# Kernel tuning notes

Hardware: AMD Instinct MI355X
Metric: run time of the kernel (lower is better)

Reference implementation:

```python
import jax, jax.numpy as jnp
import numpy as np

H = 8   # num_heads
K = 2   # num_timescales (hard-coded in module)


def _apply_rope(x, cos, sin):
    # x: [B,T,H,D]; cos/sin: [1,T,1,D/2]; interleaved even/odd pairs
    xp = x.reshape(*x.shape[:-1], -1, 2)
    xr, xi = xp[..., 0], xp[..., 1]
    rr = xr * cos - xi * sin
    ri = xr * sin + xi * cos
    return jnp.stack([rr, ri], axis=-1).reshape(x.shape)


def setup_inputs() -> dict:
    key = jax.random.key(0)
    ks = jax.random.split(key, 11)
    B, T, C = 4, 2048, 1024
    HK = H * K
    s = 0.02  # xavier-ish scale
    return {
        'x': jax.random.normal(ks[0], (B, T, C), jnp.float32),
        'mask': jnp.ones((B, T), jnp.int32),
        'Wq': jax.random.normal(ks[1], (C, C), jnp.float32) * s,
        'Wk': jax.random.normal(ks[2], (C, C), jnp.float32) * s,
        'Wv': jax.random.normal(ks[3], (C, C), jnp.float32) * s,
        'Wb': jax.random.normal(ks[4], (C, HK), jnp.float32) * s,
        'bb': jax.random.normal(ks[5], (HK,), jnp.float32) * 0.5 + 2.0,
        'Wm': jax.random.normal(ks[6], (C, HK), jnp.float32) * s,
        'bm': jax.random.normal(ks[7], (HK,), jnp.float32) * 0.1,
        'Wo': jax.random.normal(ks[8], (C, C), jnp.float32) * s,
        'bo': jnp.zeros((C,), jnp.float32),
    }


def reference(x, mask, Wq, Wk, Wv, Wb, bb, Wm, bm, Wo, bo):
    B, T, C = x.shape
    D = C // H
    q = (x @ Wq).reshape(B, T, H, D)
    k = (x @ Wk).reshape(B, T, H, D)
    v = (x @ Wv).reshape(B, T, H, D)

    # RoPE cache
    inv_freq = 1.0 / (10000.0 ** (jnp.arange(0, D, 2, dtype=jnp.float32) / D))
    freqs = jnp.arange(T, dtype=jnp.float32)[:, None] * inv_freq[None, :]  # [T,D/2]
    cos = jnp.cos(freqs)[None, :, None, :].astype(x.dtype)
    sin = jnp.sin(freqs)[None, :, None, :].astype(x.dtype)
    q = _apply_rope(q, cos, sin)
    k = _apply_rope(k, cos, sin)

    beta = jax.nn.sigmoid((x @ Wb + bb).reshape(B, T, H, K))  # [B,T,H,K]
    mix = jax.nn.softmax((x @ Wm + bm).reshape(B, T, H, K), axis=-1)

    def step(S, ins):
        # S: [B,H,K,D,D]
        q_t, k_t, v_t, b_t, m_t, mk = ins  # [B,H,D],[B,H,D],[B,H,D],[B,H,K],[B,H,K],[B]
        outer = jnp.einsum('bhd,bhe->bhde', k_t, v_t)          # [B,H,D,D]
        S_new = b_t[..., None, None] * S + outer[:, :, None]   # [B,H,K,D,D]
        S = jnp.where(mk[:, None, None, None, None] > 0, S_new, S)
        y_k = jnp.einsum('bhd,bhkde->bhke', q_t, S)            # [B,H,K,D]
        y_t = jnp.sum(y_k * m_t[..., None], axis=2)            # [B,H,D]
        y_t = jnp.where(mk[:, None, None] > 0, y_t, jnp.zeros_like(y_t))
        return S, y_t

    S0 = jnp.zeros((B, H, K, D, D), x.dtype)
    xs = (jnp.swapaxes(q, 0, 1), jnp.swapaxes(k, 0, 1), jnp.swapaxes(v, 0, 1),
          jnp.swapaxes(beta, 0, 1), jnp.swapaxes(mix, 0, 1), mask.T)
    _, ys = jax.lax.scan(step, S0, xs)           # ys: [T,B,H,D]
    y = jnp.swapaxes(ys, 0, 1).reshape(B, T, C)
    return y @ Wo + bo
```

## Files before the change

### kernel.cpp

```cpp
#include <hip/hip_runtime.h>

typedef __attribute__((ext_vector_type(4))) float f32x4;
typedef __attribute__((ext_vector_type(8))) __bf16 bf16x8;

#define T_DIM 2048
#define B_DIM 4
#define C_DIM 1024
#define H_N 8
#define D_H 128
#define M_ROWS 8192
#define MC ((size_t)M_ROWS * C_DIM)
#define LCH 64
#define NCH (T_DIM / LCH)
#define CHSZ (128 * 128)
#define SWE(r) ((((r) ^ ((r) >> 3)) & 7) << 3)

#define GLDS16(g, l) __builtin_amdgcn_global_load_lds( \
    (const __attribute__((address_space(1))) void*)(g), \
    (__attribute__((address_space(3))) void*)(l), 16, 0, 0)

__global__ void rope_table_k(float2* __restrict__ tab) {
    int idx = blockIdx.x * 256 + threadIdx.x;
    if (idx >= T_DIM * 64) return;
    int t = idx >> 6, i = idx & 63;
    float freq = expf(-(2.0f * (float)i / 128.0f) * 9.210340371976184f);
    float a = (float)t * freq;
    tab[idx] = make_float2(cosf(a), sinf(a));
}

__global__ __launch_bounds__(256) void cvt_x_k(const float* __restrict__ in,
                                               __bf16* __restrict__ out) {
    int i = blockIdx.x * 256 + threadIdx.x;
    f32x4 a = ((const f32x4*)in)[i * 2];
    f32x4 b = ((const f32x4*)in)[i * 2 + 1];
    bf16x8 o;
    o[0] = (__bf16)a.x; o[1] = (__bf16)a.y; o[2] = (__bf16)a.z; o[3] = (__bf16)a.w;
    o[4] = (__bf16)b.x; o[5] = (__bf16)b.y; o[6] = (__bf16)b.z; o[7] = (__bf16)b.w;
    ((bf16x8*)out)[i] = o;
}

__global__ __launch_bounds__(256) void wtrans_k(
    const float* __restrict__ W0, const float* __restrict__ W1,
    const float* __restrict__ W2, const float* __restrict__ W3,
    __bf16* __restrict__ out) {
    const float* W = blockIdx.z == 0 ? W0 : blockIdx.z == 1 ? W1 :
                     blockIdx.z == 2 ? W2 : W3;
    __bf16* o = out + (size_t)blockIdx.z * C_DIM * C_DIM;
    __shared__ float t[64][65];
    int tid = threadIdx.x;
    int r0 = blockIdx.y * 64, c0 = blockIdx.x * 64;
    #pragma unroll
    for (int it = 0; it < 4; ++it) {
        int idx = it * 256 + tid;
        int r = idx >> 4, c4 = (idx & 15) * 4;
        f32x4 v = *(const f32x4*)(W + (size_t)(r0 + r) * C_DIM + c0 + c4);
        t[r][c4] = v.x; t[r][c4 + 1] = v.y; t[r][c4 + 2] = v.z; t[r][c4 + 3] = v.w;
    }
    __syncthreads();
    #pragma unroll
    for (int it = 0; it < 2; ++it) {
        int idx = it * 256 + tid;
        int n = idx >> 3, k8 = (idx & 7) * 8;
        bf16x8 ov;
        #pragma unroll
        for (int j = 0; j < 8; ++j) ov[j] = (__bf16)t[k8 + j][n];
        *(bf16x8*)(o + (size_t)(c0 + n) * C_DIM + r0 + k8) = ov;
    }
}

__global__ __launch_bounds__(256) void wbm_trans_k(
    const float* __restrict__ Wb, const float* __restrict__ Wm,
    __bf16* __restrict__ WbmT) {
    int n = blockIdx.x;
    int col = n & 15;
    const float* W = (n < 16) ? Wb : Wm;
    for (int k = threadIdx.x; k < C_DIM; k += 256)
        WbmT[(size_t)n * C_DIM + k] = (__bf16)W[(size_t)k * 16 + col];
}

__global__ __launch_bounds__(256) void betamix_mfma(
    const __bf16* __restrict__ xb, const __bf16* __restrict__ WbmT,
    const float* __restrict__ bb, const float* __restrict__ bm,
    float* __restrict__ beta, float* __restrict__ mix) {
    __shared__ __bf16 As[32 * 64];

    int tid = threadIdx.x;
    int w = tid >> 6, lane = tid & 63;
    int lr = lane & 15, lg = lane >> 4;
    int ifr = w >> 1, j = w & 1;
    int rows0 = blockIdx.x * 32;

    int srow = tid >> 3;
    int sg = (tid & 7) ^ (srow & 7);
    size_t aoff = (size_t)(rows0 + srow) * C_DIM + sg * 8;
    char* ldsb = (char*)As + w * 64 * 16;

    f32x4 acc = {};
    const __bf16* Wrow = WbmT + (size_t)(j * 16 + lr) * C_DIM;

    for (int k0 = 0; k0 < C_DIM; k0 += 64) {
        __syncthreads();
        GLDS16(xb + aoff + k0, ldsb);
        __syncthreads();
        #pragma unroll
        for (int ss = 0; ss < 2; ++ss) {
            int ar = ifr * 16 + lr;
            bf16x8 af = *(const bf16x8*)((char*)As + ar * 128 + (((ss * 4 + lg) ^ (ar & 7)) << 4));
            bf16x8 bf = *(const bf16x8*)(Wrow + k0 + ss * 32 + lg * 8);
            acc = __builtin_amdgcn_mfma_f32_16x16x32_bf16(af, bf, acc, 0, 0, 0);
        }
    }

    float bias = (j ? bm : bb)[lr];
    #pragma unroll
    for (int r = 0; r < 4; ++r) {
        int row = rows0 + ifr * 16 + lg * 4 + r;
        float v = acc[r] + bias;
        if (j == 0) {
            beta[(size_t)row * 16 + lr] = 1.f / (1.f + expf(-v));
        } else {
            float other = __shfl_xor(v, 1);
            float mx = fmaxf(v, other);
            float e = expf(v - mx), eo = expf(other - mx);
            mix[(size_t)row * 16 + lr] = e / (e + eo);
        }
    }
}

template<bool ROPE, bool OUTF32>
__global__ __launch_bounds__(256) void gemm_bt(
    const __bf16* __restrict__ A, const __bf16* __restrict__ BT,
    void* __restrict__ Cp, int M, int N, int K,
    const float2* __restrict__ rope_tab, const float* __restrict__ bias) {
    __shared__ __bf16 As[128 * 64];
    __shared__ __bf16 Bs[128 * 64];

    int tid = threadIdx.x;
    int nTN = N >> 7;
    int cpx = gridDim.x >> 3;
    int bid = ((int)blockIdx.x & 7) * cpx + ((int)blockIdx.x >> 3);
    int bm = bid / nTN, bn = bid % nTN;
    int m_base = bm << 7, n_base = bn << 7;
    int w = tid >> 6, lane = tid & 63;
    int lr = lane & 15, lg = lane >> 4;
    int wm = (w >> 1) * 64, wn = (w & 1) * 64;

    size_t aoff[4], boff[4];
    int ldso[4];
    #pragma unroll
    for (int it = 0; it < 4; ++it) {
        int gi = it * 256 + tid;
        int row = gi >> 3;
        int g = (gi & 7) ^ (row & 7);
        aoff[it] = (size_t)(m_base + row) * K + g * 8;
        boff[it] = (size_t)(n_base + row) * K + g * 8;
        ldso[it] = (it * 256 + w * 64) * 16;
    }

    f32x4 acc[4][4] = {};

    for (int k0 = 0; k0 < K; k0 += 64) {
        __syncthreads();
        #pragma unroll
        for (int it = 0; it < 4; ++it) {
            GLDS16(A + aoff[it] + k0, (char*)As + ldso[it]);
            GLDS16(BT + boff[it] + k0, (char*)Bs + ldso[it]);
        }
        __syncthreads();
        #pragma unroll
        for (int ss = 0; ss < 2; ++ss) {
            bf16x8 af[4], bfr[4];
            #pragma unroll
            for (int i = 0; i < 4; ++i) {
                int ar = wm + i * 16 + lr;
                af[i] = *(const bf16x8*)((char*)As + ar * 128 + (((ss * 4 + lg) ^ (ar & 7)) << 4));
                int br = wn + i * 16 + lr;
                bfr[i] = *(const bf16x8*)((char*)Bs + br * 128 + (((ss * 4 + lg) ^ (br & 7)) << 4));
            }
            #pragma unroll
            for (int i = 0; i < 4; ++i)
                #pragma unroll
                for (int j = 0; j < 4; ++j)
                    acc[i][j] = __builtin_amdgcn_mfma_f32_16x16x32_bf16(af[i], bfr[j], acc[i][j], 0, 0, 0);
        }
    }

    #pragma unroll
    for (int i = 0; i < 4; ++i) {
        #pragma unroll
        for (int j = 0; j < 4; ++j) {
            #pragma unroll
            for (int r = 0; r < 4; ++r) {
                int grow = m_base + wm + i * 16 + (lg << 2) + r;
                int gcol = n_base + wn + j * 16 + lr;
                float val = acc[i][j][r];
                if (ROPE) {
                    float partner = __shfl_xor(val, 1);
                    int t = grow & (T_DIM - 1);
                    int ii = (gcol & 127) >> 1;
                    float2 cs = rope_tab[t * 64 + ii];
                    val = (gcol & 1) ? (partner * cs.y + val * cs.x)
                                     : (val * cs.x - partner * cs.y);
                }
                if (bias) val += bias[gcol];
                size_t idx = (size_t)grow * N + gcol;
                if (OUTF32) ((float*)Cp)[idx] = val;
                else        ((__bf16*)Cp)[idx] = (__bf16)val;
            }
        }
    }
}

__global__ __launch_bounds__(256) void chunk_sum_k(
    const __bf16* __restrict__ kg, const __bf16* __restrict__ vg,
    const float* __restrict__ beta, const int* __restrict__ mask,
    __bf16* __restrict__ BT, float* __restrict__ cumLg) {
    __shared__ __bf16 KT[128 * 64];
    __shared__ __bf16 VT[128 * 64];
    __shared__ float wvf[LCH], mkf[LCH];

    int tid = threadIdx.x;
    int c = blockIdx.x, kk = blockIdx.y, bh = blockIdx.z;
    int b = bh >> 3, h = bh & 7;
    int scan = bh * 2 + kk;
    size_t rowb = (size_t)b * T_DIM + c * LCH;

    if (tid < 64) {
        int s = tid;
        size_t row = rowb + s;
        int mk = mask[row];
        float mf = mk ? 1.f : 0.f;
        float bt = mk ? beta[row * 16 + h * 2 + kk] : 1.f;
        float cum = bt;
        #pragma unroll
        for (int off = 1; off < 64; off <<= 1) {
            float p = __shfl(cum, (s >= off) ? s - off : 0);
            if (s >= off) cum *= p;
        }
        float cl = __shfl(cum, 63);
        wvf[s] = cl / cum;
        mkf[s] = mf;
        if (s == 63) cumLg[scan * NCH + c] = cum;
    }
    __syncthreads();

    #pragma unroll
    for (int it = 0; it < 4; ++it) {
        int f = tid + it * 256;
        int s = f >> 4, c8 = (f & 15) * 8;
        size_t g = (rowb + s) * C_DIM + h * D_H + c8;
        bf16x8 kv = *(const bf16x8*)(kg + g);
        bf16x8 vv = *(const bf16x8*)(vg + g);
        float ws_ = wvf[s], mf = mkf[s];
        #pragma unroll
        for (int j = 0; j < 8; ++j) {
            int d = c8 + j;
            KT[d * 64 + (s ^ SWE(d))] = (__bf16)(ws_ * (float)kv[j]);
            VT[d * 64 + (s ^ SWE(d))] = (__bf16)(mf * (float)vv[j]);
        }
    }
    __syncthreads();

    int w = tid >> 6, l = tid & 63;
    int lr = l & 15, lg = l >> 4;
    f32x4 acc[2][8] = {};
    #pragma unroll
    for (int kt = 0; kt < 2; ++kt) {
        int col = kt * 32 + lg * 8;
        bf16x8 aV[2], bK[8];
        #pragma unroll
        for (int et = 0; et < 2; ++et) {
            int e = w * 32 + et * 16 + lr;
            aV[et] = *(const bf16x8*)&VT[e * 64 + (col ^ SWE(e))];
        }
        #pragma unroll
        for (int dt = 0; dt < 8; ++dt) {
            int d = dt * 16 + lr;
            bK[dt] = *(const bf16x8*)&KT[d * 64 + (col ^ SWE(d))];
        }
        #pragma unroll
        for (int et = 0; et < 2; ++et)
            #pragma unroll
            for (int dt = 0; dt < 8; ++dt)
                acc[et][dt] = __builtin_amdgcn_mfma_f32_16x16x32_bf16(aV[et], bK[dt], acc[et][dt], 0, 0, 0);
    }

    __bf16* bout = BT + ((size_t)scan * NCH + c) * CHSZ;
    #pragma unroll
    for (int et = 0; et < 2; ++et)
        #pragma unroll
        for (int dt = 0; dt < 8; ++dt)
            #pragma unroll
            for (int r = 0; r < 4; ++r) {
                int e = w * 32 + et * 16 + lg * 4 + r;
                bout[e * 128 + dt * 16 + lr] = (__bf16)acc[et][dt][r];
            }
}

__global__ __launch_bounds__(256) void chunk_scan_k(
    __bf16* __restrict__ BT, const float* __restrict__ cumLg) {
    int bid = blockIdx.x;
    int scan = bid >> 3, part = bid & 7;
    int tid = threadIdx.x;
    int e = part * 16 + (tid >> 4);
    int d0 = (tid & 15) * 8;
    __bf16* base = BT + (size_t)scan * NCH * CHSZ + e * 128 + d0;
    const float* cl = cumLg + scan * NCH;
    float acc[8] = {};
    for (int c = 0; c < NCH; ++c) {
        bf16x8 bv = *(const bf16x8*)(base + (size_t)c * CHSZ);
        float g = cl[c];
        bf16x8 so;
        #pragma unroll
        for (int j = 0; j < 8; ++j) so[j] = (__bf16)acc[j];
        *(bf16x8*)(base + (size_t)c * CHSZ) = so;
        #pragma unroll
        for (int j = 0; j < 8; ++j) acc[j] = g * acc[j] + (float)bv[j];
    }
}

__global__ __launch_bounds__(256) void chunk_out_k(
    const __bf16* __restrict__ qg, const __bf16* __restrict__ kg,
    const __bf16* __restrict__ vg, const __bf16* __restrict__ ST,
    const float* __restrict__ beta, const float* __restrict__ mixp,
    const int* __restrict__ mask, __bf16* __restrict__ yg) {
    __shared__ __bf16 Qs[64 * 136];
    __shared__ __bf16 Ks[64 * 136];
    __shared__ __bf16 VT[128 * 64];
    __shared__ __bf16 Ps[2][64 * 72];
    __shared__ float rcumf[2][64], qscf[2][64], mkf[64];

    int tid = threadIdx.x;
    int c = blockIdx.x, bh = blockIdx.y;
    int b = bh >> 3, h = bh & 7;
    size_t rowb = (size_t)b * T_DIM + c * LCH;

    if (tid < 128) {
        int s = tid & 63, kk = tid >> 6;
        size_t row = rowb + s;
        int mk = mask[row];
        float bt = mk ? beta[row * 16 + h * 2 + kk] : 1.f;
        float cum = bt;
        #pragma unroll
        for (int off = 1; off < 64; off <<= 1) {
            float p = __shfl(cum, (s >= off) ? s - off : 0);
            if (s >= off) cum *= p;
        }
        rcumf[kk][s] = 1.f / cum;
        qscf[kk][s] = cum * (mk ? mixp[row * 16 + h * 2 + kk] : 0.f);
        if (kk == 0) mkf[s] = mk ? 1.f : 0.f;
    }
    __syncthreads();

    #pragma unroll
    for (int it = 0; it < 4; ++it) {
        int f = tid + it * 256;
        int t = f >> 4, c8 = (f & 15) * 8;
        size_t g = (rowb + t) * C_DIM + h * D_H + c8;
        *(bf16x8*)&Qs[t * 136 + c8] = *(const bf16x8*)(qg + g);
        *(bf16x8*)&Ks[t * 136 + c8] = *(const bf16x8*)(kg + g);
    }
    #pragma unroll
    for (int it = 0; it < 4; ++it) {
        int f = tid + it * 256;
        int s = f >> 4, c8 = (f & 15) * 8;
        size_t g = (rowb + s) * C_DIM + h * D_H + c8;
        bf16x8 vv = *(const bf16x8*)(vg + g);
        float mf = mkf[s];
        #pragma unroll
        for (int j = 0; j < 8; ++j) {
            int e = c8 + j;
            VT[e * 64 + (s ^ SWE(e))] = (__bf16)(mf * (float)vv[j]);
        }
    }
    __syncthreads();

    int w = tid >> 6, l = tid & 63;
    int lr = l & 15, lg = l >> 4;

    bf16x8 aQ[4];
    #pragma unroll
    for (int kt = 0; kt < 4; ++kt)
        aQ[kt] = *(const bf16x8*)&Qs[(w * 16 + lr) * 136 + kt * 32 + lg * 8];

    f32x4 Praw[4];
    #pragma unroll
    for (int st = 0; st < 4; ++st) {
        f32x4 p = {};
        #pragma unroll
        for (int kt = 0; kt < 4; ++kt) {
            bf16x8 bk = *(const bf16x8*)&Ks[(st * 16 + lr) * 136 + kt * 32 + lg * 8];
            p = __builtin_amdgcn_mfma_f32_16x16x32_bf16(aQ[kt], bk, p, 0, 0, 0);
        }
        Praw[st] = p;
    }

    f32x4 yA[8] = {};
    #pragma unroll
    for (int kk = 0; kk < 2; ++kk) {
        #pragma unroll
        for (int st = 0; st < 4; ++st) {
            #pragma unroll
            for (int r = 0; r < 4; ++r) {
                int tl = w * 16 + lg * 4 + r;
                int sc = st * 16 + lr;
                float pv = (sc <= tl) ? Praw[st][r] * rcumf[kk][sc] * qscf[kk][tl] : 0.f;
                Ps[kk][tl * 72 + sc] = (__bf16)pv;
            }
        }
        bf16x8 aP[2];
        #pragma unroll
        for (int k2 = 0; k2 < 2; ++k2)
            aP[k2] = *(const bf16x8*)&Ps[kk][(w * 16 + lr) * 72 + k2 * 32 + lg * 8];

        const __bf16* stb = ST + ((size_t)(bh * 2 + kk) * NCH + c) * CHSZ;
        #pragma unroll
        for (int et = 0; et < 8; ++et) {
            int e = et * 16 + lr;
            f32x4 ys = {};
            #pragma unroll
            for (int kt = 0; kt < 4; ++kt) {
                bf16x8 bs = *(const bf16x8*)(stb + e * 128 + kt * 32 + lg * 8);
                ys = __builtin_amdgcn_mfma_f32_16x16x32_bf16(aQ[kt], bs, ys, 0, 0, 0);
            }
            f32x4 yp = {};
            #pragma unroll
            for (int k2 = 0; k2 < 2; ++k2) {
                bf16x8 bv = *(const bf16x8*)&VT[e * 64 + ((k2 * 32 + lg * 8) ^ SWE(e))];
                yp = __builtin_amdgcn_mfma_f32_16x16x32_bf16(aP[k2], bv, yp, 0, 0, 0);
            }
            #pragma unroll
            for (int r = 0; r < 4; ++r)
                yA[et][r] += ys[r] * qscf[kk][w * 16 + lg * 4 + r] + yp[r];
        }
    }
    #pragma unroll
    for (int et = 0; et < 8; ++et)
        #pragma unroll
        for (int r = 0; r < 4; ++r) {
            size_t row = rowb + w * 16 + lg * 4 + r;
            yg[row * C_DIM + h * D_H + et * 16 + lr] = (__bf16)yA[et][r];
        }
}

extern "C" void kernel_launch(void* const* d_in, const int* in_sizes, int n_in,
                              void* d_out, int out_size, void* d_ws, size_t ws_size,
                              hipStream_t stream) {
    const float* x    = (const float*)d_in[0];
    const int*   mask = (const int*)d_in[1];
    const float* Wq   = (const float*)d_in[2];
    const float* Wk   = (const float*)d_in[3];
    const float* Wv   = (const float*)d_in[4];
    const float* Wb   = (const float*)d_in[5];
    const float* bb   = (const float*)d_in[6];
    const float* Wm   = (const float*)d_in[7];
    const float* bm   = (const float*)d_in[8];
    const float* Wo   = (const float*)d_in[9];
    const float* bo   = (const float*)d_in[10];
    float* out = (float*)d_out;

    __bf16* q    = (__bf16*)d_ws;
    __bf16* k    = q + MC;
    __bf16* v    = k + MC;
    __bf16* xb   = v + MC;
    __bf16* WT   = xb + MC;
    __bf16* BT   = WT + (size_t)4 * C_DIM * C_DIM;
    float* beta  = (float*)(BT + (size_t)64 * NCH * CHSZ);
    float* mixb  = beta + M_ROWS * 16;
    float* cumL  = mixb + M_ROWS * 16;
    float2* rope = (float2*)(cumL + 64 * NCH);
    __bf16* WbmT = (__bf16*)(rope + T_DIM * 64);
    __bf16* ysum = xb;

    rope_table_k<<<dim3((T_DIM * 64) / 256), dim3(256), 0, stream>>>(rope);
    cvt_x_k<<<dim3(MC / 8 / 256), dim3(256), 0, stream>>>(x, xb);
    wtrans_k<<<dim3(16, 16, 4), dim3(256), 0, stream>>>(Wq, Wk, Wv, Wo, WT);
    wbm_trans_k<<<dim3(32), dim3(256), 0, stream>>>(Wb, Wm, WbmT);
    betamix_mfma<<<dim3(M_ROWS / 32), dim3(256), 0, stream>>>(xb, WbmT, bb, bm, beta, mixb);

    const size_t CC = (size_t)C_DIM * C_DIM;
    dim3 ggrid((M_ROWS / 128) * (C_DIM / 128));
    gemm_bt<true,  false><<<ggrid, dim3(256), 0, stream>>>(xb, WT,          q,   M_ROWS, C_DIM, C_DIM, rope, nullptr);
    gemm_bt<true,  false><<<ggrid, dim3(256), 0, stream>>>(xb, WT + CC,     k,   M_ROWS, C_DIM, C_DIM, rope, nullptr);
    gemm_bt<false, false><<<ggrid, dim3(256), 0, stream>>>(xb, WT + 2 * CC, v,   M_ROWS, C_DIM, C_DIM, nullptr, nullptr);

    chunk_sum_k<<<dim3(NCH, 2, 32), dim3(256), 0, stream>>>(k, v, beta, mask, BT, cumL);
    chunk_scan_k<<<dim3(512), dim3(256), 0, stream>>>(BT, cumL);
    chunk_out_k<<<dim3(NCH, 32), dim3(256), 0, stream>>>(q, k, v, BT, beta, mixb, mask, ysum);

    gemm_bt<false, true><<<ggrid, dim3(256), 0, stream>>>(ysum, WT + 3 * CC, out, M_ROWS, C_DIM, C_DIM, nullptr, bo);
}
```

Before: 245.9 us.

## Fuse Q/K/V projections into one GEMM launch and drop Q/K LDS staging

```diff
diff --git a/kernel.cpp b/kernel.cpp
--- a/kernel.cpp
+++ b/kernel.cpp
@@ -127,7 +127,7 @@
     }
 }
 
-template<bool ROPE, bool OUTF32>
+template<int MODE>
 __global__ __launch_bounds__(256) void gemm_bt(
     const __bf16* __restrict__ A, const __bf16* __restrict__ BT,
     void* __restrict__ Cp, int M, int N, int K,
@@ -194,18 +194,22 @@
                 int grow = m_base + wm + i * 16 + (lg << 2) + r;
                 int gcol = n_base + wn + j * 16 + lr;
                 float val = acc[i][j][r];
-                if (ROPE) {
-                    float partner = __shfl_xor(val, 1);
-                    int t = grow & (T_DIM - 1);
-                    int ii = (gcol & 127) >> 1;
-                    float2 cs = rope_tab[t * 64 + ii];
-                    val = (gcol & 1) ? (partner * cs.y + val * cs.x)
-                                     : (val * cs.x - partner * cs.y);
+                if (MODE == 1) {
+                    int buf = gcol >> 10;
+                    int col = gcol & 1023;
+                    if (buf < 2) {
+                        float partner = __shfl_xor(val, 1);
+                        int t = grow & (T_DIM - 1);
+                        int ii = (col & 127) >> 1;
+                        float2 cs = rope_tab[t * 64 + ii];
+                        val = (col & 1) ? (partner * cs.y + val * cs.x)
+                                        : (val * cs.x - partner * cs.y);
+                    }
+                    ((__bf16*)Cp)[(size_t)buf * MC + (size_t)grow * C_DIM + col] = (__bf16)val;
+                } else {
+                    if (bias) val += bias[gcol];
+                    ((float*)Cp)[(size_t)grow * N + gcol] = val;
                 }
-                if (bias) val += bias[gcol];
-                size_t idx = (size_t)grow * N + gcol;
-                if (OUTF32) ((float*)Cp)[idx] = val;
-                else        ((__bf16*)Cp)[idx] = (__bf16)val;
             }
         }
     }
@@ -324,10 +328,8 @@
     const __bf16* __restrict__ vg, const __bf16* __restrict__ ST,
     const float* __restrict__ beta, const float* __restrict__ mixp,
     const int* __restrict__ mask, __bf16* __restrict__ yg) {
-    __shared__ __bf16 Qs[64 * 136];
-    __shared__ __bf16 Ks[64 * 136];
     __shared__ __bf16 VT[128 * 64];
-    __shared__ __bf16 Ps[2][64 * 72];
+    __shared__ __bf16 Ps[64 * 72];
     __shared__ float rcumf[2][64], qscf[2][64], mkf[64];
 
     int tid = threadIdx.x;
@@ -355,14 +357,6 @@
     #pragma unroll
     for (int it = 0; it < 4; ++it) {
         int f = tid + it * 256;
-        int t = f >> 4, c8 = (f & 15) * 8;
-        size_t g = (rowb + t) * C_DIM + h * D_H + c8;
-        *(bf16x8*)&Qs[t * 136 + c8] = *(const bf16x8*)(qg + g);
-        *(bf16x8*)&Ks[t * 136 + c8] = *(const bf16x8*)(kg + g);
-    }
-    #pragma unroll
-    for (int it = 0; it < 4; ++it) {
-        int f = tid + it * 256;
         int s = f >> 4, c8 = (f & 15) * 8;
         size_t g = (rowb + s) * C_DIM + h * D_H + c8;
         bf16x8 vv = *(const bf16x8*)(vg + g);
@@ -378,18 +372,20 @@
     int w = tid >> 6, l = tid & 63;
     int lr = l & 15, lg = l >> 4;
 
+    const __bf16* qrow = qg + (rowb + w * 16 + lr) * C_DIM + h * D_H;
     bf16x8 aQ[4];
     #pragma unroll
     for (int kt = 0; kt < 4; ++kt)
-        aQ[kt] = *(const bf16x8*)&Qs[(w * 16 + lr) * 136 + kt * 32 + lg * 8];
-
+        aQ[kt] = *(const bf16x8*)(qrow + kt * 32 + lg * 8);
+
+    const __bf16* kbase = kg + rowb * C_DIM + h * D_H;
     f32x4 Praw[4];
     #pragma unroll
     for (int st = 0; st < 4; ++st) {
         f32x4 p = {};
         #pragma unroll
         for (int kt = 0; kt < 4; ++kt) {
-            bf16x8 bk = *(const bf16x8*)&Ks[(st * 16 + lr) * 136 + kt * 32 + lg * 8];
+            bf16x8 bk = *(const bf16x8*)(kbase + (size_t)(st * 16 + lr) * C_DIM + kt * 32 + lg * 8);
             p = __builtin_amdgcn_mfma_f32_16x16x32_bf16(aQ[kt], bk, p, 0, 0, 0);
         }
         Praw[st] = p;
@@ -405,13 +401,13 @@
                 int tl = w * 16 + lg * 4 + r;
                 int sc = st * 16 + lr;
                 float pv = (sc <= tl) ? Praw[st][r] * rcumf[kk][sc] * qscf[kk][tl] : 0.f;
-                Ps[kk][tl * 72 + sc] = (__bf16)pv;
+                Ps[tl * 72 + sc] = (__bf16)pv;
             }
         }
         bf16x8 aP[2];
         #pragma unroll
         for (int k2 = 0; k2 < 2; ++k2)
-            aP[k2] = *(const bf16x8*)&Ps[kk][(w * 16 + lr) * 72 + k2 * 32 + lg * 8];
+            aP[k2] = *(const bf16x8*)&Ps[(w * 16 + lr) * 72 + k2 * 32 + lg * 8];
 
         const __bf16* stb = ST + ((size_t)(bh * 2 + kk) * NCH + c) * CHSZ;
         #pragma unroll
@@ -479,14 +475,13 @@
     betamix_mfma<<<dim3(M_ROWS / 32), dim3(256), 0, stream>>>(xb, WbmT, bb, bm, beta, mixb);
 
     const size_t CC = (size_t)C_DIM * C_DIM;
-    dim3 ggrid((M_ROWS / 128) * (C_DIM / 128));
-    gemm_bt<true,  false><<<ggrid, dim3(256), 0, stream>>>(xb, WT,          q,   M_ROWS, C_DIM, C_DIM, rope, nullptr);
-    gemm_bt<true,  false><<<ggrid, dim3(256), 0, stream>>>(xb, WT + CC,     k,   M_ROWS, C_DIM, C_DIM, rope, nullptr);
-    gemm_bt<false, false><<<ggrid, dim3(256), 0, stream>>>(xb, WT + 2 * CC, v,   M_ROWS, C_DIM, C_DIM, nullptr, nullptr);
+    gemm_bt<1><<<dim3((M_ROWS / 128) * (3 * C_DIM / 128)), dim3(256), 0, stream>>>(
+        xb, WT, q, M_ROWS, 3 * C_DIM, C_DIM, rope, nullptr);
 
     chunk_sum_k<<<dim3(NCH, 2, 32), dim3(256), 0, stream>>>(k, v, beta, mask, BT, cumL);
     chunk_scan_k<<<dim3(512), dim3(256), 0, stream>>>(BT, cumL);
     chunk_out_k<<<dim3(NCH, 32), dim3(256), 0, stream>>>(q, k, v, BT, beta, mixb, mask, ysum);
 
-    gemm_bt<false, true><<<ggrid, dim3(256), 0, stream>>>(ysum, WT + 3 * CC, out, M_ROWS, C_DIM, C_DIM, nullptr, bo);
-}
+    gemm_bt<0><<<dim3((M_ROWS / 128) * (C_DIM / 128)), dim3(256), 0, stream>>>(
+        ysum, WT + 3 * CC, out, M_ROWS, C_DIM, C_DIM, nullptr, bo);
+}
```

After: 256.1 us. 4.2% more time.

## Double-buffer GEMM LDS tiles and load Q/K fragments directly from global

Applied to the files above, without the earlier changes.

```diff
diff --git a/kernel.cpp b/kernel.cpp
--- a/kernel.cpp
+++ b/kernel.cpp
@@ -82,7 +82,7 @@
     const __bf16* __restrict__ xb, const __bf16* __restrict__ WbmT,
     const float* __restrict__ bb, const float* __restrict__ bm,
     float* __restrict__ beta, float* __restrict__ mix) {
-    __shared__ __bf16 As[32 * 64];
+    __shared__ __bf16 As[2][32 * 64];
 
     int tid = threadIdx.x;
     int w = tid >> 6, lane = tid & 63;
@@ -93,22 +93,27 @@
     int srow = tid >> 3;
     int sg = (tid & 7) ^ (srow & 7);
     size_t aoff = (size_t)(rows0 + srow) * C_DIM + sg * 8;
-    char* ldsb = (char*)As + w * 64 * 16;
+    int ldso = w * 64 * 16;
 
     f32x4 acc = {};
     const __bf16* Wrow = WbmT + (size_t)(j * 16 + lr) * C_DIM;
 
-    for (int k0 = 0; k0 < C_DIM; k0 += 64) {
-        __syncthreads();
-        GLDS16(xb + aoff + k0, ldsb);
-        __syncthreads();
+    GLDS16(xb + aoff, (char*)As[0] + ldso);
+    asm volatile("s_waitcnt vmcnt(0)" ::: "memory");
+    __syncthreads();
+
+    for (int t = 0; t < 16; ++t) {
+        int cur = t & 1;
+        if (t < 15) GLDS16(xb + aoff + (t + 1) * 64, (char*)As[cur ^ 1] + ldso);
         #pragma unroll
         for (int ss = 0; ss < 2; ++ss) {
             int ar = ifr * 16 + lr;
-            bf16x8 af = *(const bf16x8*)((char*)As + ar * 128 + (((ss * 4 + lg) ^ (ar & 7)) << 4));
-            bf16x8 bf = *(const bf16x8*)(Wrow + k0 + ss * 32 + lg * 8);
+            bf16x8 af = *(const bf16x8*)((char*)As[cur] + ar * 128 + (((ss * 4 + lg) ^ (ar & 7)) << 4));
+            bf16x8 bf = *(const bf16x8*)(Wrow + t * 64 + ss * 32 + lg * 8);
             acc = __builtin_amdgcn_mfma_f32_16x16x32_bf16(af, bf, acc, 0, 0, 0);
         }
+        asm volatile("s_waitcnt vmcnt(0)" ::: "memory");
+        __syncthreads();
     }
 
     float bias = (j ? bm : bb)[lr];
@@ -132,8 +137,8 @@
     const __bf16* __restrict__ A, const __bf16* __restrict__ BT,
     void* __restrict__ Cp, int M, int N, int K,
     const float2* __restrict__ rope_tab, const float* __restrict__ bias) {
-    __shared__ __bf16 As[128 * 64];
-    __shared__ __bf16 Bs[128 * 64];
+    __shared__ __bf16 As[2][128 * 64];
+    __shared__ __bf16 Bs[2][128 * 64];
 
     int tid = threadIdx.x;
     int nTN = N >> 7;
@@ -157,25 +162,32 @@
         ldso[it] = (it * 256 + w * 64) * 16;
     }
 
+#define STAGE_G(bufi, k0)                                                   \
+    _Pragma("unroll")                                                       \
+    for (int it = 0; it < 4; ++it) {                                        \
+        GLDS16(A + aoff[it] + (k0), (char*)As[bufi] + ldso[it]);            \
+        GLDS16(BT + boff[it] + (k0), (char*)Bs[bufi] + ldso[it]);           \
+    }
+
     f32x4 acc[4][4] = {};
 
-    for (int k0 = 0; k0 < K; k0 += 64) {
-        __syncthreads();
-        #pragma unroll
-        for (int it = 0; it < 4; ++it) {
-            GLDS16(A + aoff[it] + k0, (char*)As + ldso[it]);
-            GLDS16(BT + boff[it] + k0, (char*)Bs + ldso[it]);
-        }
-        __syncthreads();
+    STAGE_G(0, 0);
+    asm volatile("s_waitcnt vmcnt(0)" ::: "memory");
+    __syncthreads();
+
+    int nt = K >> 6;
+    for (int t = 0; t < nt; ++t) {
+        int cur = t & 1;
+        if (t + 1 < nt) STAGE_G(cur ^ 1, (t + 1) * 64);
         #pragma unroll
         for (int ss = 0; ss < 2; ++ss) {
             bf16x8 af[4], bfr[4];
             #pragma unroll
             for (int i = 0; i < 4; ++i) {
                 int ar = wm + i * 16 + lr;
-                af[i] = *(const bf16x8*)((char*)As + ar * 128 + (((ss * 4 + lg) ^ (ar & 7)) << 4));
+                af[i] = *(const bf16x8*)((char*)As[cur] + ar * 128 + (((ss * 4 + lg) ^ (ar & 7)) << 4));
                 int br = wn + i * 16 + lr;
-                bfr[i] = *(const bf16x8*)((char*)Bs + br * 128 + (((ss * 4 + lg) ^ (br & 7)) << 4));
+                bfr[i] = *(const bf16x8*)((char*)Bs[cur] + br * 128 + (((ss * 4 + lg) ^ (br & 7)) << 4));
             }
             #pragma unroll
             for (int i = 0; i < 4; ++i)
@@ -183,7 +195,10 @@
                 for (int j = 0; j < 4; ++j)
                     acc[i][j] = __builtin_amdgcn_mfma_f32_16x16x32_bf16(af[i], bfr[j], acc[i][j], 0, 0, 0);
         }
-    }
+        asm volatile("s_waitcnt vmcnt(0)" ::: "memory");
+        __syncthreads();
+    }
+#undef STAGE_G
 
     #pragma unroll
     for (int i = 0; i < 4; ++i) {
@@ -324,10 +339,8 @@
     const __bf16* __restrict__ vg, const __bf16* __restrict__ ST,
     const float* __restrict__ beta, const float* __restrict__ mixp,
     const int* __restrict__ mask, __bf16* __restrict__ yg) {
-    __shared__ __bf16 Qs[64 * 136];
-    __shared__ __bf16 Ks[64 * 136];
     __shared__ __bf16 VT[128 * 64];
-    __shared__ __bf16 Ps[2][64 * 72];
+    __shared__ __bf16 Ps[64 * 72];
     __shared__ float rcumf[2][64], qscf[2][64], mkf[64];
 
     int tid = threadIdx.x;
@@ -355,14 +368,6 @@
     #pragma unroll
     for (int it = 0; it < 4; ++it) {
         int f = tid + it * 256;
-        int t = f >> 4, c8 = (f & 15) * 8;
-        size_t g = (rowb + t) * C_DIM + h * D_H + c8;
-        *(bf16x8*)&Qs[t * 136 + c8] = *(const bf16x8*)(qg + g);
-        *(bf16x8*)&Ks[t * 136 + c8] = *(const bf16x8*)(kg + g);
-    }
-    #pragma unroll
-    for (int it = 0; it < 4; ++it) {
-        int f = tid + it * 256;
         int s = f >> 4, c8 = (f & 15) * 8;
         size_t g = (rowb + s) * C_DIM + h * D_H + c8;
         bf16x8 vv = *(const bf16x8*)(vg + g);
@@ -378,18 +383,20 @@
     int w = tid >> 6, l = tid & 63;
     int lr = l & 15, lg = l >> 4;
 
+    const __bf16* qrow = qg + (rowb + w * 16 + lr) * C_DIM + h * D_H;
     bf16x8 aQ[4];
     #pragma unroll
     for (int kt = 0; kt < 4; ++kt)
-        aQ[kt] = *(const bf16x8*)&Qs[(w * 16 + lr) * 136 + kt * 32 + lg * 8];
-
+        aQ[kt] = *(const bf16x8*)(qrow + kt * 32 + lg * 8);
+
+    const __bf16* kbase = kg + rowb * C_DIM + h * D_H;
     f32x4 Praw[4];
     #pragma unroll
     for (int st = 0; st < 4; ++st) {
         f32x4 p = {};
         #pragma unroll
         for (int kt = 0; kt < 4; ++kt) {
-            bf16x8 bk = *(const bf16x8*)&Ks[(st * 16 + lr) * 136 + kt * 32 + lg * 8];
+            bf16x8 bk = *(const bf16x8*)(kbase + (size_t)(st * 16 + lr) * C_DIM + kt * 32 + lg * 8);
             p = __builtin_amdgcn_mfma_f32_16x16x32_bf16(aQ[kt], bk, p, 0, 0, 0);
         }
         Praw[st] = p;
@@ -405,13 +412,13 @@
                 int tl = w * 16 + lg * 4 + r;
                 int sc = st * 16 + lr;
                 float pv = (sc <= tl) ? Praw[st][r] * rcumf[kk][sc] * qscf[kk][tl] : 0.f;
-                Ps[kk][tl * 72 + sc] = (__bf16)pv;
+                Ps[tl * 72 + sc] = (__bf16)pv;
             }
         }
         bf16x8 aP[2];
         #pragma unroll
         for (int k2 = 0; k2 < 2; ++k2)
-            aP[k2] = *(const bf16x8*)&Ps[kk][(w * 16 + lr) * 72 + k2 * 32 + lg * 8];
+            aP[k2] = *(const bf16x8*)&Ps[(w * 16 + lr) * 72 + k2 * 32 + lg * 8];
 
         const __bf16* stb = ST + ((size_t)(bh * 2 + kk) * NCH + c) * CHSZ;
         #pragma unroll
```

Result: no change. 243.2 us (-1.1%).
